# Kernel optimization log

Hardware: AMD Instinct MI355X
Metric: run time of the kernel (lower is better)

## Reference

```python
import jax, jax.numpy as jnp
import numpy as np

HID = 256
N_HEADS = 4
ATTN_DIM = HID // N_HEADS  # 64
B, S = 64, 512
NEG = -1e10


def setup_inputs() -> dict:
    key = jax.random.key(0)
    ks = jax.random.split(key, 12)
    def lin(k, fan_in, shape):
        bound = 1.0 / np.sqrt(fan_in)
        return jax.random.uniform(k, shape, jnp.float32, -bound, bound)
    return {
        "query": jax.random.normal(ks[0], (B, S, HID), jnp.float32),
        "key": jax.random.normal(ks[1], (B, S, HID), jnp.float32),
        "value": jax.random.normal(ks[2], (B, S, HID), jnp.float32),
        "mask": jax.random.randint(ks[3], (B, 1, S, S), 0, 2, jnp.int32),
        "Wq": lin(ks[4], HID, (HID, HID)), "bq": lin(ks[5], HID, (HID,)),
        "Wk": lin(ks[6], HID, (HID, HID)), "bk": lin(ks[7], HID, (HID,)),
        "Wv": lin(ks[8], HID, (HID, ATTN_DIM)), "bv": lin(ks[9], HID, (ATTN_DIM,)),
        "Wh": lin(ks[10], ATTN_DIM, (ATTN_DIM, HID)), "bh": lin(ks[11], ATTN_DIM, (HID,)),
    }


def reference(query, key, value, mask, Wq, bq, Wk, bk, Wv, bv, Wh, bh):
    b = query.shape[0]
    scale = jnp.sqrt(jnp.asarray(ATTN_DIM, query.dtype))
    Q = (query @ Wq + bq).reshape(b, -1, N_HEADS, ATTN_DIM).transpose(0, 2, 1, 3)  # [B,H,Sq,d]
    K = (key @ Wk + bk).reshape(b, -1, N_HEADS, ATTN_DIM).transpose(0, 2, 1, 3)    # [B,H,Sk,d]
    V = value @ Wv + bv                                                            # [B,Sk,d]
    energy = jnp.einsum('bhqd,bhkd->bhqk', Q, K) / scale
    energy = jnp.where(mask == 0, jnp.asarray(NEG, energy.dtype), energy)
    probs = jax.nn.softmax(energy, axis=-1)          # [B,H,Sq,Sk]
    attention = jnp.mean(probs, axis=1)              # head-mean, [B,Sq,Sk]
    # dropout is identity in eval mode
    output = jnp.einsum('bqk,bkd->bqd', attention, V) @ Wh + bh  # [B,Sq,HID]
    return output, attention
```

## Files before the change

kernel.cpp:

```cpp
#include <hip/hip_runtime.h>

#define NB 64
#define SS 512
#define HIDD 256
#define NHEADS 4
#define ADIM 64
#define NTOT 576

typedef __attribute__((ext_vector_type(8))) short short8v;
typedef __attribute__((ext_vector_type(4))) float f32x4;

#define MFMA16(A, B, C) __builtin_amdgcn_mfma_f32_16x16x32_bf16(A, B, C, 0, 0, 0)
#define AS1 __attribute__((address_space(1)))
#define AS3 __attribute__((address_space(3)))

__device__ __forceinline__ void g2l16(void* lds, const void* g) {
    __builtin_amdgcn_global_load_lds((const AS1 unsigned*)g,
                                     (AS3 unsigned*)lds, 16, 0, 0);
}

__device__ __forceinline__ void bsplit(float x, short& hi, short& lo) {
    unsigned u = __float_as_uint(x);
    unsigned uh = (u + 0x8000u) & 0xFFFF0000u;
    hi = (short)(uh >> 16);
    float r = x - __uint_as_float(uh);
    lo = (short)((__float_as_uint(r) + 0x8000u) >> 16);
}

__device__ __forceinline__ void bsplit_v(float x, short8v& vh, short8v& vl, int i) {
    short h, l;
    bsplit(x, h, l);
    vh[i] = h;
    vl[i] = l;
}

__device__ __forceinline__ short bf16r(float x) {
    return (short)((__float_as_uint(x) + 0x8000u) >> 16);
}

__device__ __forceinline__ int frag_addr(int bb, int hh, int s, int d) {
    const int t16 = s >> 4, rk = s & 15;
    const int ks2 = d >> 5, lgk = (d >> 3) & 3, e8 = d & 7;
    return ((((bb * 4 + hh) * 32 + t16) * 2 + ks2) * 64 + rk + 16 * lgk) * 8 + e8;
}

__global__ __launch_bounds__(256) void prep_weights(
    const float* __restrict__ Wq, const float* __restrict__ Wk,
    const float* __restrict__ Wv, const float* __restrict__ Wh,
    short* __restrict__ WT_hi, short* __restrict__ WT_lo,
    short* __restrict__ WhT)
{
    const int bx = blockIdx.x;
    if (bx < NTOT) {
        const int idx = bx * 256 + threadIdx.x;
        const int n = idx >> 8, k = idx & 255;
        float v;
        if (n < 256)      v = Wq[k * 256 + n];
        else if (n < 512) v = Wk[k * 256 + (n - 256)];
        else              v = Wv[k * 64 + (n - 512)];
        short h, l;
        bsplit(v, h, l);
        WT_hi[idx] = h;
        WT_lo[idx] = l;
    } else {
        const int idx2 = (bx - NTOT) * 256 + threadIdx.x;
        const int n = idx2 >> 6, d = idx2 & 63;
        WhT[idx2] = bf16r(Wh[d * HIDD + n]);
    }
}

__global__ __launch_bounds__(256) void qkv_qk(
    const float* __restrict__ query, const float* __restrict__ key,
    const short* __restrict__ WT_hi, const short* __restrict__ WT_lo,
    const float* __restrict__ bq, const float* __restrict__ bk,
    short* __restrict__ Qhi, short* __restrict__ Khi)
{
    __shared__ short Ws_h[2][256 * 32];
    __shared__ short Ws_l[2][256 * 32];

    const int bm = blockIdx.x * 64;
    const int y = blockIdx.y;
    const int nrow0 = y << 8;
    const float* A = y ? key : query;
    const float* biasp = y ? bk : bq;
    short* Dhi = y ? Khi : Qhi;

    const int tid = threadIdx.x;
    const int w = tid >> 6, l = tid & 63;
    const int l15 = l & 15, lg = l >> 4;
    const int wbase = tid & 192;

    auto stageWT = [&](int buf, int kc) {
#pragma unroll
        for (int i = 0; i < 4; ++i) {
            const int g = i * 256 + tid;
            const int row = g >> 2;
            const int p = g & 3;
            const int sl = p ^ (row & 3);
            const size_t goff = (size_t)(nrow0 + row) * HIDD + kc * 32 + sl * 8;
            g2l16(&Ws_h[buf][(i * 256 + wbase) * 8], WT_hi + goff);
            g2l16(&Ws_l[buf][(i * 256 + wbase) * 8], WT_lo + goff);
        }
    };

    const float* arow = A + (size_t)(bm + w * 16 + l15) * HIDD + lg * 8;

    f32x4 acc[16];
#pragma unroll
    for (int jn = 0; jn < 16; ++jn) acc[jn] = (f32x4){0.f, 0.f, 0.f, 0.f};

    float4 a0c = *reinterpret_cast<const float4*>(arow);
    float4 a1c = *reinterpret_cast<const float4*>(arow + 4);
    stageWT(0, 0);
    __syncthreads();

    int cur = 0;
#pragma unroll
    for (int kc = 0; kc < 8; ++kc) {
        float4 a0n, a1n;
        if (kc < 7) {
            a0n = *reinterpret_cast<const float4*>(arow + (kc + 1) * 32);
            a1n = *reinterpret_cast<const float4*>(arow + (kc + 1) * 32 + 4);
            stageWT(cur ^ 1, kc + 1);
        }

        short8v ah, al;
        bsplit_v(a0c.x, ah, al, 0);
        bsplit_v(a0c.y, ah, al, 1);
        bsplit_v(a0c.z, ah, al, 2);
        bsplit_v(a0c.w, ah, al, 3);
        bsplit_v(a1c.x, ah, al, 4);
        bsplit_v(a1c.y, ah, al, 5);
        bsplit_v(a1c.z, ah, al, 6);
        bsplit_v(a1c.w, ah, al, 7);

#pragma unroll
        for (int jn = 0; jn < 16; ++jn) {
            const int rowB = jn * 16 + l15;
            const int c = lg ^ (rowB & 3);
            short8v bh = *reinterpret_cast<const short8v*>(&Ws_h[cur][rowB * 32 + c * 8]);
            short8v bl = *reinterpret_cast<const short8v*>(&Ws_l[cur][rowB * 32 + c * 8]);
            acc[jn] = MFMA16(ah, bh, acc[jn]);
            acc[jn] = MFMA16(ah, bl, acc[jn]);
            acc[jn] = MFMA16(al, bh, acc[jn]);
        }
        __syncthreads();
        cur ^= 1;
        if (kc < 7) { a0c = a0n; a1c = a1n; }
    }

#pragma unroll
    for (int jn = 0; jn < 16; ++jn) {
        const int ncol = jn * 16 + l15;
        const float bias = biasp[ncol];
        const int hh = ncol >> 6, dd = ncol & 63;
#pragma unroll
        for (int r = 0; r < 4; ++r) {
            const int m = bm + w * 16 + lg * 4 + r;
            const int bb = m >> 9, s = m & 511;
            const int fa = frag_addr(bb, hh, s, dd);
            Dhi[fa] = bf16r(acc[jn][r] + bias);
        }
    }
}

__global__ __launch_bounds__(256) void qkv_v(
    const float* __restrict__ value,
    const short* __restrict__ WT_hi, const short* __restrict__ WT_lo,
    const float* __restrict__ bv, short* __restrict__ VT)
{
    __shared__ short Ws_h[2][64 * 32];
    __shared__ short Ws_l[2][64 * 32];

    const int bm = blockIdx.x * 64;
    const int tid = threadIdx.x;
    const int w = tid >> 6, l = tid & 63;
    const int l15 = l & 15, lg = l >> 4;
    const int wbase = tid & 192;

    auto stageWT = [&](int buf, int kc) {
        const int row = tid >> 2;
        const int p = tid & 3;
        const int sl = p ^ (row & 3);
        const size_t goff = (size_t)(512 + row) * HIDD + kc * 32 + sl * 8;
        g2l16(&Ws_h[buf][wbase * 8], WT_hi + goff);
        g2l16(&Ws_l[buf][wbase * 8], WT_lo + goff);
    };

    const float* arow = value + (size_t)(bm + w * 16 + l15) * HIDD + lg * 8;

    f32x4 acc[4];
#pragma unroll
    for (int jn = 0; jn < 4; ++jn) acc[jn] = (f32x4){0.f, 0.f, 0.f, 0.f};

    float4 a0c = *reinterpret_cast<const float4*>(arow);
    float4 a1c = *reinterpret_cast<const float4*>(arow + 4);
    stageWT(0, 0);
    __syncthreads();

    int cur = 0;
#pragma unroll
    for (int kc = 0; kc < 8; ++kc) {
        float4 a0n, a1n;
        if (kc < 7) {
            a0n = *reinterpret_cast<const float4*>(arow + (kc + 1) * 32);
            a1n = *reinterpret_cast<const float4*>(arow + (kc + 1) * 32 + 4);
            stageWT(cur ^ 1, kc + 1);
        }

        short8v ah, al;
        bsplit_v(a0c.x, ah, al, 0);
        bsplit_v(a0c.y, ah, al, 1);
        bsplit_v(a0c.z, ah, al, 2);
        bsplit_v(a0c.w, ah, al, 3);
        bsplit_v(a1c.x, ah, al, 4);
        bsplit_v(a1c.y, ah, al, 5);
        bsplit_v(a1c.z, ah, al, 6);
        bsplit_v(a1c.w, ah, al, 7);

#pragma unroll
        for (int jn = 0; jn < 4; ++jn) {
            const int rowB = jn * 16 + l15;
            const int c = lg ^ (rowB & 3);
            short8v bh = *reinterpret_cast<const short8v*>(&Ws_h[cur][rowB * 32 + c * 8]);
            short8v bl = *reinterpret_cast<const short8v*>(&Ws_l[cur][rowB * 32 + c * 8]);
            acc[jn] = MFMA16(ah, bh, acc[jn]);
            acc[jn] = MFMA16(ah, bl, acc[jn]);
            acc[jn] = MFMA16(al, bh, acc[jn]);
        }
        __syncthreads();
        cur ^= 1;
        if (kc < 7) { a0c = a0n; a1c = a1n; }
    }

#pragma unroll
    for (int jn = 0; jn < 4; ++jn) {
        const int d = jn * 16 + l15;
        const float bias = bv[d];
#pragma unroll
        for (int r = 0; r < 4; ++r) {
            const int m = bm + w * 16 + lg * 4 + r;
            const int bb = m >> 9, kk = m & 511;
            const int ks = kk >> 5;
            const int lane = l15 + 16 * ((kk >> 3) & 3);
            const int idx = (((bb * 4 + jn) * 16 + ks) * 64 + lane) * 8 + (kk & 7);
            VT[idx] = bf16r(acc[jn][r] + bias);
        }
    }
}

__global__ __launch_bounds__(512) void attn_probs_fused(
    const short* __restrict__ Qhi_g, const short* __restrict__ Khi_g,
    const short* __restrict__ VT, const short* __restrict__ WhT,
    const int* __restrict__ mask, const float* __restrict__ bh,
    float* __restrict__ attn, float* __restrict__ out)
{
    __shared__ __align__(16) short P_s[32 * 512];
    __shared__ float red[2][8][2][16];

    const int wg = blockIdx.x;
    const int swz = (wg & 7) * 128 + (wg >> 3);
    const int b = swz >> 4;
    const int q0 = (swz & 15) * 32;

    const int tid = threadIdx.x;
    const int w = tid >> 6;
    const int h2 = w >> 2;
    const int sp = w & 3;
    const int l = tid & 63;
    const int l15 = l & 15;
    const int lg = l >> 4;

    unsigned mbits[2];
#pragma unroll
    for (int qs = 0; qs < 2; ++qs) {
        unsigned bits = 0;
        const int q = q0 + qs * 16 + l15;
        const int* mrow = mask + ((size_t)b * SS + q) * SS;
#pragma unroll
        for (int kl = 0; kl < 2; ++kl)
#pragma unroll
            for (int ms = 0; ms < 2; ++ms) {
                const int fi = kl * 2 + ms;
                const int kt = 2 * h2 + kl;
                const int k = kt * 128 + (2 * sp + ms) * 16 + lg * 4;
                int4 mv = *reinterpret_cast<const int4*>(&mrow[k]);
                bits |= (mv.x != 0 ? 1u : 0u) << (fi * 4 + 0);
                bits |= (mv.y != 0 ? 1u : 0u) << (fi * 4 + 1);
                bits |= (mv.z != 0 ? 1u : 0u) << (fi * 4 + 2);
                bits |= (mv.w != 0 ? 1u : 0u) << (fi * 4 + 3);
            }
        mbits[qs] = bits;
    }

    f32x4 acc[2][2][2];
#pragma unroll
    for (int kl = 0; kl < 2; ++kl)
#pragma unroll
        for (int ms = 0; ms < 2; ++ms)
#pragma unroll
            for (int qs = 0; qs < 2; ++qs)
                acc[kl][ms][qs] = (f32x4){0.f, 0.f, 0.f, 0.f};

    const int qt_base = (swz & 15) * 2;

    for (int h = 0; h < NHEADS; ++h) {
        const int bh32 = (b * 4 + h) * 32;

        short8v qh[2][2];
#pragma unroll
        for (int ks2 = 0; ks2 < 2; ++ks2)
#pragma unroll
            for (int qs = 0; qs < 2; ++qs) {
                const int off = (((bh32 + qt_base + qs) * 2 + ks2) * 64 + l) * 8;
                qh[ks2][qs] = *reinterpret_cast<const short8v*>(Qhi_g + off);
            }

        f32x4 e[2][2][2];
#pragma unroll
        for (int kl = 0; kl < 2; ++kl)
#pragma unroll
            for (int ms = 0; ms < 2; ++ms)
#pragma unroll
                for (int qs = 0; qs < 2; ++qs)
                    e[kl][ms][qs] = (f32x4){0.f, 0.f, 0.f, 0.f};

#pragma unroll
        for (int kl = 0; kl < 2; ++kl) {
            const int t0 = (2 * h2 + kl) * 8 + 2 * sp;
#pragma unroll
            for (int ks2 = 0; ks2 < 2; ++ks2) {
                const int base0 = (((bh32 + t0) * 2 + ks2) * 64 + l) * 8;
                const int base1 = base0 + 1024;
                short8v ah0 = *reinterpret_cast<const short8v*>(Khi_g + base0);
                short8v ah1 = *reinterpret_cast<const short8v*>(Khi_g + base1);

                e[kl][0][0] = MFMA16(ah0, qh[ks2][0], e[kl][0][0]);
                e[kl][0][1] = MFMA16(ah0, qh[ks2][1], e[kl][0][1]);
                e[kl][1][0] = MFMA16(ah1, qh[ks2][0], e[kl][1][0]);
                e[kl][1][1] = MFMA16(ah1, qh[ks2][1], e[kl][1][1]);
            }
        }

        float sm[2] = {0.f, 0.f};
        const float c = 0.125f;
#pragma unroll
        for (int kl = 0; kl < 2; ++kl)
#pragma unroll
            for (int ms = 0; ms < 2; ++ms)
#pragma unroll
                for (int qs = 0; qs < 2; ++qs)
#pragma unroll
                    for (int r = 0; r < 4; ++r) {
                        float p = __expf(e[kl][ms][qs][r] * c);
                        const unsigned bit = (mbits[qs] >> ((kl * 2 + ms) * 4 + r)) & 1u;
                        p = bit ? p : 0.f;
                        e[kl][ms][qs][r] = p;
                        sm[qs] += p;
                    }
#pragma unroll
        for (int qs = 0; qs < 2; ++qs) {
            sm[qs] += __shfl_xor(sm[qs], 16);
            sm[qs] += __shfl_xor(sm[qs], 32);
        }
        if (l < 16) { red[h & 1][w][0][l] = sm[0]; red[h & 1][w][1][l] = sm[1]; }
        __syncthreads();
#pragma unroll
        for (int qs = 0; qs < 2; ++qs) {
            float Z = 0.f;
#pragma unroll
            for (int wv = 0; wv < 8; ++wv) Z += red[h & 1][wv][qs][l15];
            const float inv = 0.25f / fmaxf(Z, 1e-30f);
#pragma unroll
            for (int kl = 0; kl < 2; ++kl)
#pragma unroll
                for (int ms = 0; ms < 2; ++ms)
#pragma unroll
                    for (int r = 0; r < 4; ++r)
                        acc[kl][ms][qs][r] += e[kl][ms][qs][r] * inv;
        }
    }

#pragma unroll
    for (int kl = 0; kl < 2; ++kl)
#pragma unroll
        for (int ms = 0; ms < 2; ++ms)
#pragma unroll
            for (int qs = 0; qs < 2; ++qs) {
                const int kt = 2 * h2 + kl;
                const int q = q0 + qs * 16 + l15;
                const int k = kt * 128 + (2 * sp + ms) * 16 + lg * 4;
                float4 o;
                o.x = acc[kl][ms][qs][0];
                o.y = acc[kl][ms][qs][1];
                o.z = acc[kl][ms][qs][2];
                o.w = acc[kl][ms][qs][3];
                *reinterpret_cast<float4*>(&attn[((size_t)b * SS + q) * SS + k]) = o;

                const int ql_ = qs * 16 + l15;
                const int c8 = kt * 16 + (2 * sp + ms) * 2 + (lg >> 1);
                const int phys = c8 ^ (ql_ & 7);
                short4 pk;
                pk.x = bf16r(acc[kl][ms][qs][0]);
                pk.y = bf16r(acc[kl][ms][qs][1]);
                pk.z = bf16r(acc[kl][ms][qs][2]);
                pk.w = bf16r(acc[kl][ms][qs][3]);
                *reinterpret_cast<short4*>(&P_s[ql_ * 512 + phys * 8 + (lg & 1) * 4]) = pk;
            }
    __syncthreads();

    f32x4 tacc[2];
    tacc[0] = (f32x4){0.f, 0.f, 0.f, 0.f};
    tacc[1] = (f32x4){0.f, 0.f, 0.f, 0.f};
    if (w < 4) {
#pragma unroll
        for (int ks = 0; ks < 16; ++ks) {
            short8v va = *reinterpret_cast<const short8v*>(
                VT + (((b * 4 + w) * 16 + ks) * 64 + l) * 8);
#pragma unroll
            for (int qt = 0; qt < 2; ++qt) {
                const int q = qt * 16 + l15;
                const int phys = (ks * 4 + lg) ^ (q & 7);
                short8v pb = *reinterpret_cast<const short8v*>(&P_s[q * 512 + phys * 8]);
                tacc[qt] = MFMA16(va, pb, tacc[qt]);
            }
        }
    }
    __syncthreads();

    float* T_s = reinterpret_cast<float*>(P_s);
    if (w < 4) {
#pragma unroll
        for (int qt = 0; qt < 2; ++qt) {
            const int q = qt * 16 + l15;
            const int d = w * 16 + lg * 4;
            float4 tv;
            tv.x = tacc[qt][0];
            tv.y = tacc[qt][1];
            tv.z = tacc[qt][2];
            tv.w = tacc[qt][3];
            *reinterpret_cast<float4*>(&T_s[q * 68 + d]) = tv;
        }
    }
    __syncthreads();

    if (w < 4) {
        f32x4 oacc[2][4];
#pragma unroll
        for (int qt = 0; qt < 2; ++qt)
#pragma unroll
            for (int nt = 0; nt < 4; ++nt)
                oacc[qt][nt] = (f32x4){0.f, 0.f, 0.f, 0.f};

#pragma unroll
        for (int ks = 0; ks < 2; ++ks) {
            short8v ta[2];
#pragma unroll
            for (int qt = 0; qt < 2; ++qt) {
                const int q = qt * 16 + l15;
                float4 t0 = *reinterpret_cast<const float4*>(&T_s[q * 68 + ks * 32 + lg * 8]);
                float4 t1 = *reinterpret_cast<const float4*>(&T_s[q * 68 + ks * 32 + lg * 8 + 4]);
                ta[qt][0] = bf16r(t0.x);
                ta[qt][1] = bf16r(t0.y);
                ta[qt][2] = bf16r(t0.z);
                ta[qt][3] = bf16r(t0.w);
                ta[qt][4] = bf16r(t1.x);
                ta[qt][5] = bf16r(t1.y);
                ta[qt][6] = bf16r(t1.z);
                ta[qt][7] = bf16r(t1.w);
            }
#pragma unroll
            for (int nt = 0; nt < 4; ++nt) {
                const int n = (w * 4 + nt) * 16 + l15;
                short8v wb = *reinterpret_cast<const short8v*>(
                    WhT + n * 64 + ks * 32 + lg * 8);
#pragma unroll
                for (int qt = 0; qt < 2; ++qt)
                    oacc[qt][nt] = MFMA16(ta[qt], wb, oacc[qt][nt]);
            }
        }

#pragma unroll
        for (int qt = 0; qt < 2; ++qt)
#pragma unroll
            for (int nt = 0; nt < 4; ++nt) {
                const int n = (w * 4 + nt) * 16 + l15;
                const float bias = bh[n];
#pragma unroll
                for (int r = 0; r < 4; ++r) {
                    const int q = q0 + qt * 16 + lg * 4 + r;
                    out[((size_t)b * SS + q) * HIDD + n] = oacc[qt][nt][r] + bias;
                }
            }
    }
}

extern "C" void kernel_launch(void* const* d_in, const int* in_sizes, int n_in,
                              void* d_out, int out_size, void* d_ws, size_t ws_size,
                              hipStream_t stream)
{
    const float* query = (const float*)d_in[0];
    const float* key   = (const float*)d_in[1];
    const float* value = (const float*)d_in[2];
    const int*   mask  = (const int*)d_in[3];
    const float* Wq = (const float*)d_in[4];
    const float* bq = (const float*)d_in[5];
    const float* Wk = (const float*)d_in[6];
    const float* bk = (const float*)d_in[7];
    const float* Wv = (const float*)d_in[8];
    const float* bv = (const float*)d_in[9];
    const float* Wh = (const float*)d_in[10];
    const float* bh = (const float*)d_in[11];

    float* out  = (float*)d_out;
    float* attn = out + (size_t)NB * SS * HIDD;

    const size_t BS = (size_t)NB * SS;
    short* Qhi = (short*)d_ws;
    short* Khi = Qhi + BS * HIDD;
    short* VT  = Khi + BS * HIDD;
    short* WhT = VT + BS * ADIM;

    short* WT_hi = (short*)attn;
    short* WT_lo = WT_hi + NTOT * HIDD;

    prep_weights<<<dim3(NTOT + 64), 256, 0, stream>>>(Wq, Wk, Wv, Wh,
                                                      WT_hi, WT_lo, WhT);
    qkv_qk<<<dim3(512, 2), 256, 0, stream>>>(query, key, WT_hi, WT_lo,
                                             bq, bk, Qhi, Khi);
    qkv_v<<<dim3(512), 256, 0, stream>>>(value, WT_hi, WT_lo, bv, VT);
    attn_probs_fused<<<dim3(1024), 512, 0, stream>>>(Qhi, Khi, VT, WhT,
                                                     mask, bh, attn, out);
}
```

Before: 138.8 us.

## Pre-swizzle projection weights into MFMA fragment layout and load directly from global

The weight prep kernel now writes the bf16 hi/lo split weights in MFMA B-fragment order. The QKV projection kernels then read each fragment with one contiguous 16-byte global load per lane, instead of staging tiles through double-buffered LDS with global_load_lds and barriers. This removes LDS traffic, the swizzle arithmetic and the per-k-chunk __syncthreads. In exchange, every wave re-reads the weights from L2/L1 rather than sharing one staged copy, so global load latency is exposed inside the MFMA loop with no explicit prefetch.

```diff
diff --git a/kernel.cpp b/kernel.cpp
--- a/kernel.cpp
+++ b/kernel.cpp
@@ -11,13 +11,6 @@
 typedef __attribute__((ext_vector_type(4))) float f32x4;
 
 #define MFMA16(A, B, C) __builtin_amdgcn_mfma_f32_16x16x32_bf16(A, B, C, 0, 0, 0)
-#define AS1 __attribute__((address_space(1)))
-#define AS3 __attribute__((address_space(3)))
-
-__device__ __forceinline__ void g2l16(void* lds, const void* g) {
-    __builtin_amdgcn_global_load_lds((const AS1 unsigned*)g,
-                                     (AS3 unsigned*)lds, 16, 0, 0);
-}
 
 __device__ __forceinline__ void bsplit(float x, short& hi, short& lo) {
     unsigned u = __float_as_uint(x);
@@ -44,10 +37,16 @@
     return ((((bb * 4 + hh) * 32 + t16) * 2 + ks2) * 64 + rk + 16 * lgk) * 8 + e8;
 }
 
+__device__ __forceinline__ int wtf_addr(int n, int k) {
+    const int nt = n >> 4, rn = n & 15;
+    const int kc = k >> 5, lgk = (k >> 3) & 3, e8 = k & 7;
+    return ((nt * 8 + kc) * 64 + rn + 16 * lgk) * 8 + e8;
+}
+
 __global__ __launch_bounds__(256) void prep_weights(
     const float* __restrict__ Wq, const float* __restrict__ Wk,
     const float* __restrict__ Wv, const float* __restrict__ Wh,
-    short* __restrict__ WT_hi, short* __restrict__ WT_lo,
+    short* __restrict__ WTf_hi, short* __restrict__ WTf_lo,
     short* __restrict__ WhT)
 {
     const int bx = blockIdx.x;
@@ -60,8 +59,9 @@
         else              v = Wv[k * 64 + (n - 512)];
         short h, l;
         bsplit(v, h, l);
-        WT_hi[idx] = h;
-        WT_lo[idx] = l;
+        const int fa = wtf_addr(n, k);
+        WTf_hi[fa] = h;
+        WTf_lo[fa] = l;
     } else {
         const int idx2 = (bx - NTOT) * 256 + threadIdx.x;
         const int n = idx2 >> 6, d = idx2 & 63;
@@ -71,16 +71,13 @@
 
 __global__ __launch_bounds__(256) void qkv_qk(
     const float* __restrict__ query, const float* __restrict__ key,
-    const short* __restrict__ WT_hi, const short* __restrict__ WT_lo,
+    const short* __restrict__ WTf_hi, const short* __restrict__ WTf_lo,
     const float* __restrict__ bq, const float* __restrict__ bk,
     short* __restrict__ Qhi, short* __restrict__ Khi)
 {
-    __shared__ short Ws_h[2][256 * 32];
-    __shared__ short Ws_l[2][256 * 32];
-
     const int bm = blockIdx.x * 64;
     const int y = blockIdx.y;
-    const int nrow0 = y << 8;
+    const int nt0 = y << 4;
     const float* A = y ? key : query;
     const float* biasp = y ? bk : bq;
     short* Dhi = y ? Khi : Qhi;
@@ -88,20 +85,6 @@
     const int tid = threadIdx.x;
     const int w = tid >> 6, l = tid & 63;
     const int l15 = l & 15, lg = l >> 4;
-    const int wbase = tid & 192;
-
-    auto stageWT = [&](int buf, int kc) {
-#pragma unroll
-        for (int i = 0; i < 4; ++i) {
-            const int g = i * 256 + tid;
-            const int row = g >> 2;
-            const int p = g & 3;
-            const int sl = p ^ (row & 3);
-            const size_t goff = (size_t)(nrow0 + row) * HIDD + kc * 32 + sl * 8;
-            g2l16(&Ws_h[buf][(i * 256 + wbase) * 8], WT_hi + goff);
-            g2l16(&Ws_l[buf][(i * 256 + wbase) * 8], WT_lo + goff);
-        }
-    };
 
     const float* arow = A + (size_t)(bm + w * 16 + l15) * HIDD + lg * 8;
 
@@ -111,17 +94,13 @@
 
     float4 a0c = *reinterpret_cast<const float4*>(arow);
     float4 a1c = *reinterpret_cast<const float4*>(arow + 4);
-    stageWT(0, 0);
-    __syncthreads();
-
-    int cur = 0;
+
 #pragma unroll
     for (int kc = 0; kc < 8; ++kc) {
         float4 a0n, a1n;
         if (kc < 7) {
             a0n = *reinterpret_cast<const float4*>(arow + (kc + 1) * 32);
             a1n = *reinterpret_cast<const float4*>(arow + (kc + 1) * 32 + 4);
-            stageWT(cur ^ 1, kc + 1);
         }
 
         short8v ah, al;
@@ -136,16 +115,13 @@
 
 #pragma unroll
         for (int jn = 0; jn < 16; ++jn) {
-            const int rowB = jn * 16 + l15;
-            const int c = lg ^ (rowB & 3);
-            short8v bh = *reinterpret_cast<const short8v*>(&Ws_h[cur][rowB * 32 + c * 8]);
-            short8v bl = *reinterpret_cast<const short8v*>(&Ws_l[cur][rowB * 32 + c * 8]);
+            const int base = (((nt0 + jn) * 8 + kc) * 64 + l) * 8;
+            short8v bh = *reinterpret_cast<const short8v*>(WTf_hi + base);
+            short8v bl = *reinterpret_cast<const short8v*>(WTf_lo + base);
             acc[jn] = MFMA16(ah, bh, acc[jn]);
             acc[jn] = MFMA16(ah, bl, acc[jn]);
             acc[jn] = MFMA16(al, bh, acc[jn]);
         }
-        __syncthreads();
-        cur ^= 1;
         if (kc < 7) { a0c = a0n; a1c = a1n; }
     }
 
@@ -166,26 +142,13 @@
 
 __global__ __launch_bounds__(256) void qkv_v(
     const float* __restrict__ value,
-    const short* __restrict__ WT_hi, const short* __restrict__ WT_lo,
+    const short* __restrict__ WTf_hi, const short* __restrict__ WTf_lo,
     const float* __restrict__ bv, short* __restrict__ VT)
 {
-    __shared__ short Ws_h[2][64 * 32];
-    __shared__ short Ws_l[2][64 * 32];
-
     const int bm = blockIdx.x * 64;
     const int tid = threadIdx.x;
     const int w = tid >> 6, l = tid & 63;
     const int l15 = l & 15, lg = l >> 4;
-    const int wbase = tid & 192;
-
-    auto stageWT = [&](int buf, int kc) {
-        const int row = tid >> 2;
-        const int p = tid & 3;
-        const int sl = p ^ (row & 3);
-        const size_t goff = (size_t)(512 + row) * HIDD + kc * 32 + sl * 8;
-        g2l16(&Ws_h[buf][wbase * 8], WT_hi + goff);
-        g2l16(&Ws_l[buf][wbase * 8], WT_lo + goff);
-    };
 
     const float* arow = value + (size_t)(bm + w * 16 + l15) * HIDD + lg * 8;
 
@@ -195,17 +158,13 @@
 
     float4 a0c = *reinterpret_cast<const float4*>(arow);
     float4 a1c = *reinterpret_cast<const float4*>(arow + 4);
-    stageWT(0, 0);
-    __syncthreads();
-
-    int cur = 0;
+
 #pragma unroll
     for (int kc = 0; kc < 8; ++kc) {
         float4 a0n, a1n;
         if (kc < 7) {
             a0n = *reinterpret_cast<const float4*>(arow + (kc + 1) * 32);
             a1n = *reinterpret_cast<const float4*>(arow + (kc + 1) * 32 + 4);
-            stageWT(cur ^ 1, kc + 1);
         }
 
         short8v ah, al;
@@ -220,16 +179,13 @@
 
 #pragma unroll
         for (int jn = 0; jn < 4; ++jn) {
-            const int rowB = jn * 16 + l15;
-            const int c = lg ^ (rowB & 3);
-            short8v bh = *reinterpret_cast<const short8v*>(&Ws_h[cur][rowB * 32 + c * 8]);
-            short8v bl = *reinterpret_cast<const short8v*>(&Ws_l[cur][rowB * 32 + c * 8]);
+            const int base = (((32 + jn) * 8 + kc) * 64 + l) * 8;
+            short8v bh = *reinterpret_cast<const short8v*>(WTf_hi + base);
+            short8v bl = *reinterpret_cast<const short8v*>(WTf_lo + base);
             acc[jn] = MFMA16(ah, bh, acc[jn]);
             acc[jn] = MFMA16(ah, bl, acc[jn]);
             acc[jn] = MFMA16(al, bh, acc[jn]);
         }
-        __syncthreads();
-        cur ^= 1;
         if (kc < 7) { a0c = a0n; a1c = a1n; }
     }
 
@@ -521,14 +477,14 @@
     short* VT  = Khi + BS * HIDD;
     short* WhT = VT + BS * ADIM;
 
-    short* WT_hi = (short*)attn;
-    short* WT_lo = WT_hi + NTOT * HIDD;
+    short* WTf_hi = (short*)attn;
+    short* WTf_lo = WTf_hi + NTOT * HIDD;
 
     prep_weights<<<dim3(NTOT + 64), 256, 0, stream>>>(Wq, Wk, Wv, Wh,
-                                                      WT_hi, WT_lo, WhT);
-    qkv_qk<<<dim3(512, 2), 256, 0, stream>>>(query, key, WT_hi, WT_lo,
+                                                      WTf_hi, WTf_lo, WhT);
+    qkv_qk<<<dim3(512, 2), 256, 0, stream>>>(query, key, WTf_hi, WTf_lo,
                                              bq, bk, Qhi, Khi);
-    qkv_v<<<dim3(512), 256, 0, stream>>>(value, WT_hi, WT_lo, bv, VT);
+    qkv_v<<<dim3(512), 256, 0, stream>>>(value, WTf_hi, WTf_lo, bv, VT);
     attn_probs_fused<<<dim3(1024), 512, 0, stream>>>(Qhi, Khi, VT, WhT,
                                                      mask, bh, attn, out);
 }
```

Result: slower. 187.1 us (+34.8%).
